# Performance work log

Hardware: AMD Instinct MI355X
Metric: run time of the kernel (lower is better)

Reference implementation:

```python
import jax, jax.numpy as jnp
import numpy as np
from jax.scipy.linalg import expm

B, S, D, E, K, NROT = 2, 2048, 1024, 8, 2, 3
EPS = 1e-5


def setup_inputs() -> dict:
    key = jax.random.key(0)
    ks = jax.random.split(key, 16)
    sc = 0.02
    x = jax.random.normal(ks[0], (B, S, D), jnp.float32)
    ln_gamma = 1.0 + sc * jax.random.normal(ks[1], (D,), jnp.float32)
    ln_beta = sc * jax.random.normal(ks[2], (D,), jnp.float32)
    abel_w = sc * jax.random.normal(ks[3], (D, D), jnp.float32)
    abel_b = sc * jax.random.normal(ks[4], (D,), jnp.float32)
    moe_gate_w = sc * jax.random.normal(ks[5], (D, E), jnp.float32)
    moe_gate_b = sc * jax.random.normal(ks[6], (E,), jnp.float32)
    ew1 = sc * jax.random.normal(ks[7], (E, D, 2 * D), jnp.float32)
    eb1 = sc * jax.random.normal(ks[8], (E, 2 * D), jnp.float32)
    ew2 = sc * jax.random.normal(ks[9], (E, 2 * D, D), jnp.float32)
    eb2 = sc * jax.random.normal(ks[10], (E, D), jnp.float32)
    g = sc * jax.random.normal(ks[11], (NROT, D, D), jnp.float32)
    gens = 0.5 * (g - jnp.swapaxes(g, -1, -2))  # skew-symmetric, as in reset_parameters
    gc_w = sc * jax.random.normal(ks[12], (2 * D, 1), jnp.float32)
    gc_b = sc * jax.random.normal(ks[13], (1,), jnp.float32)
    return dict(x=x, ln_gamma=ln_gamma, ln_beta=ln_beta, abel_w=abel_w, abel_b=abel_b,
                moe_gate_w=moe_gate_w, moe_gate_b=moe_gate_b, ew1=ew1, eb1=eb1,
                ew2=ew2, eb2=eb2, gens=gens, gc_w=gc_w, gc_b=gc_b)


def _gelu(x):
    return jax.nn.gelu(x, approximate=False)  # torch nn.GELU default = exact erf


def _forward(x, ln_gamma, ln_beta, abel_w, abel_b, moe_gate_w, moe_gate_b,
             ew1, eb1, ew2, eb2, gens, gc_w, gc_b):
    residual = x
    # LayerNorm
    mu = jnp.mean(x, axis=-1, keepdims=True)
    var = jnp.mean((x - mu) ** 2, axis=-1, keepdims=True)
    xn = (x - mu) * jax.lax.rsqrt(var + EPS) * ln_gamma + ln_beta
    # abel branch: Linear + GELU
    abel_out = _gelu(xn @ abel_w + abel_b)
    # MoE: dense all-experts compute, masked by top-k softmax weights
    logits = xn @ moe_gate_w + moe_gate_b                      # [B,S,E]
    topw, topi = jax.lax.top_k(logits, K)                      # [B,S,K]
    topw = jax.nn.softmax(topw, axis=-1)
    w_dense = jnp.sum(jax.nn.one_hot(topi, E, dtype=xn.dtype) * topw[..., None], axis=-2)  # [B,S,E]
    h = _gelu(jnp.einsum('bsd,edh->ebsh', xn, ew1) + eb1[:, None, None, :])  # [E,B,S,2D]
    eo = jnp.einsum('ebsh,ehd->ebsd', h, ew2) + eb2[:, None, None, :]        # [E,B,S,D]
    moe_out = jnp.einsum('ebsd,bse->bsd', eo, w_dense)
    # GeometricRotation: sequential matrix_exp rotations
    for i in range(NROT):
        moe_out = moe_out @ expm(gens[i])
    # gated residual mix
    combined = jnp.concatenate([abel_out, moe_out], axis=-1)
    gate = jax.nn.sigmoid(combined @ gc_w + gc_b)              # [B,S,1]
    mixed = abel_out * (1.0 - gate) + moe_out * gate
    return residual + mixed


def reference(x, ln_gamma, ln_beta, abel_w, abel_b, moe_gate_w, moe_gate_b,
              ew1, eb1, ew2, eb2, gens, gc_w, gc_b):
    return _forward(x, ln_gamma, ln_beta, abel_w, abel_b, moe_gate_w, moe_gate_b,
                    ew1, eb1, ew2, eb2, gens, gc_w, gc_b)
```

## Files before the change

### kernel.cpp

```cpp
#include <hip/hip_runtime.h>
#include <hip/hip_bf16.h>
#include <cstdint>
#include <cstddef>

#define DD   1024
#define DD2  2048
#define EE   8
#define NTOK 4096
#define CAPR 9216
#define MAXT 72

typedef __bf16 bf16_t;
typedef __bf16 bf16x8 __attribute__((ext_vector_type(8)));
typedef __bf16 bf16x4 __attribute__((ext_vector_type(4)));
typedef float  f32x4v __attribute__((ext_vector_type(4)));

__device__ __forceinline__ float gelu_f(float v){
  const float t = v*(0.7978845608028654f + 0.0356774081f*v*v);
  const float u = __expf(2.0f*t);
  return __fdividef(v*u, 1.0f + u);
}

__device__ __forceinline__ void gload_lds16(const void* g, void* l){
  __builtin_amdgcn_global_load_lds(
    (const __attribute__((address_space(1))) unsigned int*)(uintptr_t)g,
    (__attribute__((address_space(3))) unsigned int*)(uintptr_t)l,
    16, 0, 0);
}

enum { EPI_GELU_F32=0, EPI_GELU_BF16=1, EPI_BIAS_BF16=2, EPI_SCALE_BF16=3,
       EPI_ADDV_BF16=4, EPI_BF16=5, EPI_F32=6 };

template<int BM,int BN,int EPI,bool TAB>
__global__ __launch_bounds__(256)
void gemm_bt(const bf16_t* __restrict__ A, const bf16_t* __restrict__ Bt,
             const int N, const int K, const int gx, const int gy, const int gz,
             const long sAz, const long sBz, const long sOz,
             const int* __restrict__ tileE, const int* __restrict__ tileR,
             const int* __restrict__ ntp, const int* __restrict__ offp,
             const int* __restrict__ tokOf,
             const float* __restrict__ bias, const long sBias,
             const float alpha,
             const bf16_t* __restrict__ addv,
             float* __restrict__ outF, bf16_t* __restrict__ outB)
{
  constexpr int BK = 32;
  constexpr int WM = BM/2, WN = BN/2;
  constexpr int FM = WM/16, FN = WN/16;
  constexpr int IA = BM/64, IB = BN/64;
  constexpr int NLD = IA + IB;
  __shared__ alignas(16) bf16_t sA[3][BM*BK];
  __shared__ alignas(16) bf16_t sB[3][BN*BK];

  int bx, by, bz; long ro = 0;
  if constexpr (TAB) {
    const int nwg = gx * gy;
    const int q = nwg >> 3, r = nwg & 7;
    const int k = blockIdx.x & 7, i = blockIdx.x >> 3;
    if (i >= q + (k < r ? 1 : 0)) return;
    const int l = k * q + (k < r ? k : r) + i;
    const int ti = l / gx; bx = l - ti*gx;
    if (ti >= ntp[0]) return;
    bz = tileE[ti]; by = 0;
    ro = (long)offp[bz] + tileR[ti];
  } else {
    const int nwg = gx * gy * gz;
    const int q = nwg >> 3, r = nwg & 7;
    const int k = blockIdx.x & 7, i = blockIdx.x >> 3;
    if (i >= q + (k < r ? 1 : 0)) return;
    const int l = k * q + (k < r ? k : r) + i;
    bx = l % gx; const int t2 = l / gx; by = t2 % gy; bz = t2 / gy;
  }

  const int z = bz;
  const bf16_t* Bp = Bt + (size_t)z * sBz;
  float*  oF = outF;
  bf16_t* oB = outB;
  if constexpr (TAB) {
    oB += ro * (long)N;
  } else {
    A += (size_t)z * sAz;
    if (oF) oF += (size_t)z * sOz;
    if (oB) oB += (size_t)z * sOz;
  }
  const float*  bp = bias ? bias + (size_t)z * sBias : nullptr;
  const bf16_t* vp = addv ? addv + (size_t)z * sOz   : nullptr;

  const int tid = threadIdx.x;
  const int wid = tid >> 6, lid = tid & 63;
  const int wr = wid >> 1, wc = wid & 1;
  const int brow = by * BM, bcol = bx * BN;
  const int fr = lid & 15, fq = lid >> 4;
  const int rl = lid >> 2, qs = lid & 3;

  const char* aSrc[IA];
  const char* bSrc[IB];
  #pragma unroll
  for (int i = 0; i < IA; i++) {
    const int rloc = (wid*IA + i)*16 + rl;
    const int q = qs ^ ((rloc >> 1) & 3);
    const bf16_t* arow;
    if constexpr (TAB) {
      arow = tokOf ? (A + (size_t)tokOf[ro + rloc] * K)
                   : (A + (size_t)(ro + rloc) * K);
    } else {
      arow = A + (size_t)(brow + rloc) * K;
    }
    aSrc[i] = (const char*)arow + q*16;
  }
  #pragma unroll
  for (int i = 0; i < IB; i++) {
    const int rloc = (wid*IB + i)*16 + rl;
    const int q = qs ^ ((rloc >> 1) & 3);
    bSrc[i] = (const char*)(Bp + (size_t)(bcol + rloc) * K) + q*16;
  }

  f32x4v acc[FM][FN] = {};

  auto stage = [&](int buf, int kt) {
    #pragma unroll
    for (int i = 0; i < IA; i++)
      gload_lds16(aSrc[i] + (size_t)kt*2, (char*)sA[buf] + (wid*IA + i)*1024);
    #pragma unroll
    for (int i = 0; i < IB; i++)
      gload_lds16(bSrc[i] + (size_t)kt*2, (char*)sB[buf] + (wid*IB + i)*1024);
  };

  stage(0, 0);
  stage(1, BK);
  const int nk = K / BK;
  int b0 = 0, b1 = 1, b2 = 2;

  for (int t = 0; t < nk; ++t) {
    if (t < nk - 1) asm volatile("s_waitcnt vmcnt(%0)" :: "i"(NLD) : "memory");
    else            asm volatile("s_waitcnt vmcnt(0)" ::: "memory");
    __builtin_amdgcn_s_barrier();
    __builtin_amdgcn_sched_barrier(0);
    if (t + 2 < nk) stage(b2, (t + 2)*BK);

    bf16x8 af[FM], bb[FN];
    #pragma unroll
    for (int mi = 0; mi < FM; mi++) {
      const int r2 = wr*WM + mi*16 + fr;
      const int q = fq ^ ((r2 >> 1) & 3);
      af[mi] = *(const bf16x8*)((const char*)sA[b0] + r2*64 + q*16);
    }
    #pragma unroll
    for (int ni = 0; ni < FN; ni++) {
      const int r2 = wc*WN + ni*16 + fr;
      const int q = fq ^ ((r2 >> 1) & 3);
      bb[ni] = *(const bf16x8*)((const char*)sB[b0] + r2*64 + q*16);
    }
    #pragma unroll
    for (int mi = 0; mi < FM; mi++)
      #pragma unroll
      for (int ni = 0; ni < FN; ni++)
        acc[mi][ni] = __builtin_amdgcn_mfma_f32_16x16x32_bf16(
            af[mi], bb[ni], acc[mi][ni], 0, 0, 0);

    const int tb_ = b0; b0 = b1; b1 = b2; b2 = tb_;
  }

  #pragma unroll
  for (int mi = 0; mi < FM; mi++) {
    #pragma unroll
    for (int ni = 0; ni < FN; ni++) {
      const int rg0 = brow + wr*WM + mi*16 + fq*4;
      const int cg  = bcol + wc*WN + ni*16 + fr;
      #pragma unroll
      for (int i = 0; i < 4; i++) {
        const int rg = rg0 + i;
        float v = acc[mi][ni][i];
        if constexpr (EPI == EPI_GELU_F32) {
          v += bp[cg];
          oF[(size_t)rg*N + cg] = gelu_f(v);
        } else if constexpr (EPI == EPI_GELU_BF16) {
          v += bp[cg];
          oB[(size_t)rg*N + cg] = (bf16_t)gelu_f(v);
        } else if constexpr (EPI == EPI_BIAS_BF16) {
          v += bp[cg];
          oB[(size_t)rg*N + cg] = (bf16_t)v;
        } else if constexpr (EPI == EPI_SCALE_BF16) {
          oB[(size_t)rg*N + cg] = (bf16_t)(v * alpha);
        } else if constexpr (EPI == EPI_ADDV_BF16) {
          oB[(size_t)rg*N + cg] = (bf16_t)(v + (float)vp[(size_t)rg*N + cg]);
        } else if constexpr (EPI == EPI_BF16) {
          oB[(size_t)rg*N + cg] = (bf16_t)v;
        } else {
          oF[(size_t)rg*N + cg] = v;
        }
      }
    }
  }
}

__global__ __launch_bounds__(256)
void tcvt_kernel(const float* __restrict__ src, bf16_t* __restrict__ dst, int R, int C){
  __shared__ float t[64][65];
  const size_t bo = (size_t)blockIdx.z * R * C;
  const int c0 = blockIdx.x*64, r0 = blockIdx.y*64;
  const int lx = threadIdx.x & 15, ly = threadIdx.x >> 4;
  #pragma unroll
  for (int i = 0; i < 4; i++) {
    const int row = r0 + ly + i*16;
    const float4 v = *(const float4*)(src + bo + (size_t)row*C + c0 + lx*4);
    t[ly + i*16][lx*4+0] = v.x; t[ly + i*16][lx*4+1] = v.y;
    t[ly + i*16][lx*4+2] = v.z; t[ly + i*16][lx*4+3] = v.w;
  }
  __syncthreads();
  #pragma unroll
  for (int i = 0; i < 4; i++) {
    const int c = c0 + ly + i*16;
    bf16x4 o;
    #pragma unroll
    for (int j = 0; j < 4; j++) o[j] = (bf16_t)t[lx*4+j][ly + i*16];
    *(bf16x4*)(dst + bo + (size_t)c*R + r0 + lx*4) = o;
  }
}

__global__ __launch_bounds__(256)
void tb16_kernel(const bf16_t* __restrict__ Ut, bf16_t* __restrict__ Tb){
  __shared__ bf16_t tile[32][33];
  const bf16_t* src = Ut + (size_t)(1 - blockIdx.z) * DD * DD;
  bf16_t*       dst = Tb + (size_t)blockIdx.z * DD * DD;
  const int c0 = blockIdx.x*32, r0 = blockIdx.y*32;
  #pragma unroll
  for (int i = 0; i < 4; i++)
    tile[threadIdx.y + i*8][threadIdx.x] = src[(size_t)(r0 + threadIdx.y + i*8)*DD + c0 + threadIdx.x];
  __syncthreads();
  #pragma unroll
  for (int i = 0; i < 4; i++)
    dst[(size_t)(c0 + threadIdx.y + i*8)*DD + r0 + threadIdx.x] = tile[threadIdx.x][threadIdx.y + i*8];
}

__global__ __launch_bounds__(256)
void cvt_kernel(const float* __restrict__ in, bf16_t* __restrict__ o, long n, float scale){
  const long i = ((long)blockIdx.x*256 + threadIdx.x)*4;
  if (i >= n) return;
  const float4 v = *(const float4*)(in + i);
  bf16x4 b; b[0]=(bf16_t)(v.x*scale); b[1]=(bf16_t)(v.y*scale);
  b[2]=(bf16_t)(v.z*scale); b[3]=(bf16_t)(v.w*scale);
  *(bf16x4*)(o + i) = b;
}

__global__ __launch_bounds__(256)
void vw_kernel(const bf16_t* __restrict__ Hn, const bf16_t* __restrict__ H2,
               bf16_t* __restrict__ Vb, bf16_t* __restrict__ Wtb){
  const long i0 = ((long)blockIdx.x*256 + threadIdx.x)*4;
  const long rc = i0 % (long)(DD*DD);
  const int r = (int)(rc / DD), c0 = (int)(rc % DD);
  const bf16x4 h  = *(const bf16x4*)(Hn + i0);
  const bf16x4 h2 = *(const bf16x4*)(H2 + i0);
  bf16x4 v, w;
  #pragma unroll
  for (int j = 0; j < 4; j++) {
    const float d  = (r == c0 + j) ? 1.0f : 0.0f;
    const float fh = (float)h[j], f2 = (float)h2[j];
    v[j] = (bf16_t)(d + fh + f2*0.5f);
    w[j] = (bf16_t)(d*(1.0f/6.0f) - fh*(1.0f/24.0f) + f2*(1.0f/120.0f));
  }
  *(bf16x4*)(Vb  + i0) = v;
  *(bf16x4*)(Wtb + i0) = w;
}

__global__ __launch_bounds__(256)
void ln_gate_kernel(const float* __restrict__ x, const float* __restrict__ gamma,
                    const float* __restrict__ beta, const float* __restrict__ gw,
                    const float* __restrict__ gb,
                    bf16_t* __restrict__ xnb, int2* __restrict__ ids,
                    float2* __restrict__ wts)
{
  const int t = blockIdx.x, tid = threadIdx.x, j0 = tid*4;
  const int wid = tid >> 6, lid = tid & 63;
  const float4 v = *(const float4*)(x + (size_t)t*DD + j0);
  float s  = v.x + v.y + v.z + v.w;
  float ss = v.x*v.x + v.y*v.y + v.z*v.z + v.w*v.w;
  #pragma unroll
  for (int off = 32; off; off >>= 1) { s += __shfl_down(s, off); ss += __shfl_down(ss, off); }
  __shared__ float redS[4], redQ[4], mv[2];
  if (lid == 0) { redS[wid] = s; redQ[wid] = ss; }
  __syncthreads();
  if (tid == 0) {
    const float S1 = redS[0]+redS[1]+redS[2]+redS[3];
    const float S2 = redQ[0]+redQ[1]+redQ[2]+redQ[3];
    const float mu  = S1 * (1.0f/DD);
    const float var = S2 * (1.0f/DD) - mu*mu;
    mv[0] = mu; mv[1] = rsqrtf(var + 1e-5f);
  }
  __syncthreads();
  const float mu = mv[0], rstd = mv[1];
  const float4 g = *(const float4*)(gamma + j0);
  const float4 b = *(const float4*)(beta  + j0);
  float xn[4];
  xn[0] = (v.x-mu)*rstd*g.x + b.x;
  xn[1] = (v.y-mu)*rstd*g.y + b.y;
  xn[2] = (v.z-mu)*rstd*g.z + b.z;
  xn[3] = (v.w-mu)*rstd*g.w + b.w;
  bf16x4 ov; ov[0]=(bf16_t)xn[0]; ov[1]=(bf16_t)xn[1]; ov[2]=(bf16_t)xn[2]; ov[3]=(bf16_t)xn[3];
  *(bf16x4*)(xnb + (size_t)t*DD + j0) = ov;

  float p[8] = {0,0,0,0,0,0,0,0};
  #pragma unroll
  for (int i = 0; i < 4; i++) {
    const float4 a0 = *(const float4*)(gw + (size_t)(j0+i)*EE);
    const float4 a1 = *(const float4*)(gw + (size_t)(j0+i)*EE + 4);
    const float xv = xn[i];
    p[0]+=xv*a0.x; p[1]+=xv*a0.y; p[2]+=xv*a0.z; p[3]+=xv*a0.w;
    p[4]+=xv*a1.x; p[5]+=xv*a1.y; p[6]+=xv*a1.z; p[7]+=xv*a1.w;
  }
  #pragma unroll
  for (int off = 32; off; off >>= 1) {
    #pragma unroll
    for (int e = 0; e < 8; e++) p[e] += __shfl_down(p[e], off);
  }
  __shared__ float pr[32];
  if (lid == 0) {
    #pragma unroll
    for (int e = 0; e < 8; e++) pr[wid*8 + e] = p[e];
  }
  __syncthreads();
  if (tid == 0) {
    float l[8];
    #pragma unroll
    for (int e = 0; e < 8; e++) l[e] = pr[e] + pr[8+e] + pr[16+e] + pr[24+e] + gb[e];
    int i1 = 0; float m1 = l[0];
    #pragma unroll
    for (int e = 1; e < 8; e++) if (l[e] > m1) { m1 = l[e]; i1 = e; }
    int i2 = 0; float m2 = -1e30f;
    #pragma unroll
    for (int e = 0; e < 8; e++) if (e != i1 && l[e] > m2) { m2 = l[e]; i2 = e; }
    const float wa = 1.0f/(1.0f + expf(m2 - m1));
    ids[t] = make_int2(i1, i2);
    wts[t] = make_float2(wa, 1.0f - wa);
  }
}

__global__ __launch_bounds__(256)
void route_kernel(const int2* __restrict__ ids, int* __restrict__ slotA,
                  int* __restrict__ slotB, int* __restrict__ cnt,
                  int* __restrict__ off, int* __restrict__ tileE,
                  int* __restrict__ tileR, int* __restrict__ ntp)
{
  const int tid = threadIdx.x;
  const int wid = tid >> 6, lid = tid & 63;
  __shared__ int wsum[EE][4];
  __shared__ int base[EE];
  if (tid < EE) base[tid] = 0;
  __syncthreads();
  const unsigned long long lt = (1ull << lid) - 1ull;
  for (int c0 = 0; c0 < NTOK; c0 += 256) {
    const int t = c0 + tid;
    const int2 id = ids[t];
    int pA = 0, pB = 0;
    #pragma unroll
    for (int e = 0; e < EE; e++) {
      const bool fA = (id.x == e), fB = (id.y == e);
      const unsigned long long mA = __ballot(fA);
      const unsigned long long mB = __ballot(fB);
      const int cA = __popcll(mA);
      if (lid == 0) wsum[e][wid] = cA + __popcll(mB);
      if (fA) pA = __popcll(mA & lt);
      if (fB) pB = cA + __popcll(mB & lt);
    }
    __syncthreads();
    int wbA = base[id.x], wbB = base[id.y];
    for (int w = 0; w < wid; w++) { wbA += wsum[id.x][w]; wbB += wsum[id.y][w]; }
    slotA[t] = wbA + pA;
    slotB[t] = wbB + pB;
    __syncthreads();
    if (tid < EE) base[tid] += wsum[tid][0]+wsum[tid][1]+wsum[tid][2]+wsum[tid][3];
    __syncthreads();
  }
  if (tid == 0) {
    int a = 0, nt = 0;
    for (int e = 0; e < EE; e++) {
      cnt[e] = base[e]; off[e] = a;
      for (int r2 = 0; r2 < base[e]; r2 += 128) { tileE[nt] = e; tileR[nt] = r2; nt++; }
      a += (base[e] + 127) & ~127;
    }
    ntp[0] = nt;
  }
}

__global__ __launch_bounds__(256)
void fill_tok_kernel(const int2* __restrict__ ids, const int* __restrict__ slotA,
                     const int* __restrict__ slotB, const int* __restrict__ off,
                     int* __restrict__ tokOf){
  const int t = blockIdx.x*256 + threadIdx.x;
  const int2 id = ids[t];
  tokOf[off[id.x] + slotA[t]] = t;
  tokOf[off[id.y] + slotB[t]] = t;
}

__global__ __launch_bounds__(256)
void combine_kernel(const bf16_t* __restrict__ Yg, const int2* __restrict__ ids,
                    const int* __restrict__ slotA, const int* __restrict__ slotB,
                    const int* __restrict__ off, const float2* __restrict__ wts,
                    bf16_t* __restrict__ Xa){
  const int t = blockIdx.x, j = threadIdx.x*4;
  const int2 id = ids[t];
  const float2 w = wts[t];
  const bf16x4 a = *(const bf16x4*)(Yg + (size_t)(off[id.x] + slotA[t])*DD + j);
  const bf16x4 b = *(const bf16x4*)(Yg + (size_t)(off[id.y] + slotB[t])*DD + j);
  bf16x4 o;
  #pragma unroll
  for (int i = 0; i < 4; i++) o[i] = (bf16_t)(w.x*(float)a[i] + w.y*(float)b[i]);
  *(bf16x4*)(Xa + (size_t)t*DD + j) = o;
}

__global__ __launch_bounds__(256)
void mix_kernel(const float* __restrict__ x, const bf16_t* __restrict__ abel,
                const float* __restrict__ rot, const float* __restrict__ gcw,
                const float* __restrict__ gcb, float* __restrict__ out)
{
  const int t = blockIdx.x, tid = threadIdx.x, j0 = tid*4;
  const int wid = tid >> 6, lid = tid & 63;
  const bf16x4 ab = *(const bf16x4*)(abel + (size_t)t*DD + j0);
  const float4 r  = *(const float4*)(rot  + (size_t)t*DD + j0);
  const float4 ga = *(const float4*)(gcw + j0);
  const float4 gr = *(const float4*)(gcw + DD + j0);
  const float a0 = (float)ab[0], a1 = (float)ab[1], a2 = (float)ab[2], a3 = (float)ab[3];
  float p = a0*ga.x + a1*ga.y + a2*ga.z + a3*ga.w
          + r.x*gr.x + r.y*gr.y + r.z*gr.z + r.w*gr.w;
  #pragma unroll
  for (int off = 32; off; off >>= 1) p += __shfl_down(p, off);
  __shared__ float red[4];
  __shared__ float gsh;
  if (lid == 0) red[wid] = p;
  __syncthreads();
  if (tid == 0) {
    const float P = red[0] + red[1] + red[2] + red[3] + gcb[0];
    gsh = 1.0f/(1.0f + expf(-P));
  }
  __syncthreads();
  const float gate = gsh, g1 = 1.0f - gate;
  const float4 xv = *(const float4*)(x + (size_t)t*DD + j0);
  float4 o;
  o.x = xv.x + a0*g1 + r.x*gate;
  o.y = xv.y + a1*g1 + r.y*gate;
  o.z = xv.z + a2*g1 + r.z*gate;
  o.w = xv.w + a3*g1 + r.w*gate;
  *(float4*)(out + (size_t)t*DD + j0) = o;
}

extern "C" void kernel_launch(void* const* d_in, const int* in_sizes, int n_in,
                              void* d_out, int out_size, void* d_ws, size_t ws_size,
                              hipStream_t stream)
{
  (void)in_sizes; (void)n_in; (void)out_size; (void)ws_size;
  const float* x      = (const float*)d_in[0];
  const float* ln_g   = (const float*)d_in[1];
  const float* ln_b   = (const float*)d_in[2];
  const float* abel_w = (const float*)d_in[3];
  const float* abel_b = (const float*)d_in[4];
  const float* gate_w = (const float*)d_in[5];
  const float* gate_b = (const float*)d_in[6];
  const float* ew1    = (const float*)d_in[7];
  const float* eb1    = (const float*)d_in[8];
  const float* ew2    = (const float*)d_in[9];
  const float* eb2    = (const float*)d_in[10];
  const float* gens   = (const float*)d_in[11];
  const float* gc_w   = (const float*)d_in[12];
  const float* gc_b   = (const float*)d_in[13];
  float* out = (float*)d_out;

  char* wsp = (char*)d_ws;
  auto alloc = [&](size_t bytes) -> char* {
    char* p = wsp; wsp += (bytes + 255) & ~(size_t)255; return p;
  };
  const size_t MB = 1u<<20;
  bf16_t* xnb   = (bf16_t*)alloc((size_t)NTOK*DD*2);
  int2*   ids   = (int2*)  alloc((size_t)NTOK*8);
  float2* wts   = (float2*)alloc((size_t)NTOK*8);
  int*    slotA = (int*)   alloc((size_t)NTOK*4);
  int*    slotB = (int*)   alloc((size_t)NTOK*4);
  int*    cnt   = (int*)   alloc(64);
  int*    off   = (int*)   alloc(64);
  int*    tileE = (int*)   alloc(MAXT*4);
  int*    tileR = (int*)   alloc(MAXT*4);
  int*    ntp   = (int*)   alloc(64);
  int*    tokOf = (int*)   alloc((size_t)CAPR*4);
  bf16_t* abel_wT = (bf16_t*)alloc((size_t)DD*DD*2);
  char*   UN      = alloc(64*MB);
  bf16_t* ew1T  = (bf16_t*)UN;
  bf16_t* ew2T  = (bf16_t*)(UN + 32*MB);
  bf16_t* Hn    = (bf16_t*)alloc((size_t)3*DD*DD*2);
  bf16_t* abelo = (bf16_t*)alloc((size_t)NTOK*DD*2);
  bf16_t* Yg    = (bf16_t*)alloc((size_t)CAPR*DD*2);
  bf16_t* Hg    = (bf16_t*)alloc((size_t)CAPR*DD2*2);
  bf16_t* Xa    = (bf16_t*)alloc((size_t)NTOK*DD*2);
  float*  rot   = (float*)Hg;
  bf16_t* H2  = (bf16_t*)(UN + 0*MB);
  bf16_t* H3  = (bf16_t*)(UN + 6*MB);
  bf16_t* Vb  = (bf16_t*)(UN + 12*MB);
  bf16_t* Wtb = (bf16_t*)(UN + 18*MB);
  bf16_t* Ut  = (bf16_t*)(UN + 24*MB);
  bf16_t* Tb  = (bf16_t*)(UN + 30*MB);
  bf16_t* Pb  = (bf16_t*)(UN + 34*MB);
  bf16_t* Rt  = (bf16_t*)(UN + 36*MB);
  const long D2 = (long)DD*DD;

  auto gflat = [](int gx, int gy, int gz) {
    const int nwg = gx*gy*gz; return 8 * ((nwg + 7) / 8);
  };

  tcvt_kernel<<<dim3(DD/64,  DD/64, 1),  256, 0, stream>>>(abel_w, abel_wT, DD,  DD);
  tcvt_kernel<<<dim3(DD2/64, DD/64, EE), 256, 0, stream>>>(ew1,    ew1T,    DD,  DD2);
  tcvt_kernel<<<dim3(DD/64,  DD2/64,EE), 256, 0, stream>>>(ew2,    ew2T,    DD2, DD);
  cvt_kernel<<<dim3(3*DD*DD/1024,1,1), 256, 0, stream>>>(gens, Hn, (long)3*DD*DD, -1.0f);
  hipMemsetAsync(tokOf, 0, (size_t)CAPR*4, stream);

  ln_gate_kernel<<<dim3(NTOK,1,1), 256, 0, stream>>>(x, ln_g, ln_b, gate_w, gate_b,
                                                     xnb, ids, wts);
  route_kernel<<<dim3(1,1,1), 256, 0, stream>>>(ids, slotA, slotB, cnt, off,
                                                tileE, tileR, ntp);
  fill_tok_kernel<<<dim3(NTOK/256,1,1), 256, 0, stream>>>(ids, slotA, slotB, off, tokOf);

  gemm_bt<128,128,EPI_GELU_BF16,true><<<dim3((DD2/128)*MAXT,1,1), 256, 0, stream>>>(
      xnb, ew1T, DD2, DD, DD2/128, MAXT, 1, 0, (long)DD2*DD, 0,
      tileE, tileR, ntp, off, tokOf, eb1, DD2, 1.0f, nullptr, nullptr, Hg);
  gemm_bt<128,128,EPI_BIAS_BF16,true><<<dim3((DD/128)*MAXT,1,1), 256, 0, stream>>>(
      Hg, ew2T, DD, DD2, DD/128, MAXT, 1, 0, (long)DD*DD2, 0,
      tileE, tileR, ntp, off, nullptr, eb2, DD, 1.0f, nullptr, nullptr, Yg);
  combine_kernel<<<dim3(NTOK,1,1), 256, 0, stream>>>(Yg, ids, slotA, slotB, off, wts, Xa);

  gemm_bt<128,128,EPI_GELU_BF16,false><<<dim3(gflat(8,32,1),1,1), 256, 0, stream>>>(
      xnb, abel_wT, DD, DD, 8, 32, 1, 0, 0, 0, nullptr, nullptr, nullptr, nullptr,
      nullptr, abel_b, 0, 1.0f, nullptr, nullptr, abelo);

  gemm_bt<128,128,EPI_SCALE_BF16,false><<<dim3(gflat(8,8,3),1,1), 256, 0, stream>>>(
      Hn, Hn, DD, DD, 8, 8, 3, D2, D2, D2, nullptr, nullptr, nullptr, nullptr,
      nullptr, nullptr, 0, -1.0f, nullptr, nullptr, H2);
  gemm_bt<128,128,EPI_SCALE_BF16,false><<<dim3(gflat(8,8,3),1,1), 256, 0, stream>>>(
      H2, Hn, DD, DD, 8, 8, 3, D2, D2, D2, nullptr, nullptr, nullptr, nullptr,
      nullptr, nullptr, 0, -1.0f, nullptr, nullptr, H3);
  vw_kernel<<<dim3(3*DD*DD/1024,1,1), 256, 0, stream>>>(Hn, H2, Vb, Wtb);
  gemm_bt<128,128,EPI_ADDV_BF16,false><<<dim3(gflat(8,8,3),1,1), 256, 0, stream>>>(
      H3, Wtb, DD, DD, 8, 8, 3, D2, D2, D2, nullptr, nullptr, nullptr, nullptr,
      nullptr, nullptr, 0, 1.0f, Vb, nullptr, Ut);
  tb16_kernel<<<dim3(32,32,2), dim3(32,8,1), 0, stream>>>(Ut, Tb);
  gemm_bt<64,64,EPI_BF16,false><<<dim3(gflat(16,16,1),1,1), 256, 0, stream>>>(
      Ut + 2*D2, Tb, DD, DD, 16, 16, 1, 0, 0, 0, nullptr, nullptr, nullptr, nullptr,
      nullptr, nullptr, 0, 1.0f, nullptr, nullptr, Pb);
  gemm_bt<64,64,EPI_BF16,false><<<dim3(gflat(16,16,1),1,1), 256, 0, stream>>>(
      Pb, Tb + D2, DD, DD, 16, 16, 1, 0, 0, 0, nullptr, nullptr, nullptr, nullptr,
      nullptr, nullptr, 0, 1.0f, nullptr, nullptr, Rt);
  gemm_bt<128,128,EPI_F32,false><<<dim3(gflat(8,32,1),1,1), 256, 0, stream>>>(
      Xa, Rt, DD, DD, 8, 32, 1, 0, 0, 0, nullptr, nullptr, nullptr, nullptr,
      nullptr, nullptr, 0, 1.0f, nullptr, rot, nullptr);

  mix_kernel<<<dim3(NTOK,1,1), 256, 0, stream>>>(x, abelo, rot, gc_w, gc_b, out);
}
```

Baseline: 339.1 us.

## Fuse weight prep launches, fold tokOf zeroing, shrink rotation GEMM tiles

Merges the three transpose-convert launches and the generator conversion into one prep kernel, cutting launch count and tail gaps. Replaces the full tokOf memset by zeroing only the padding slots inside fill_tok_kernel. Switches the three batched 1024x1024 generator-power GEMMs from 128x128 to 64x64 tiles, so each launches 768 workgroups instead of 192 and fills the CUs better, at the cost of less data reuse per tile. Padding slots not covered by any expert's aligned range are no longer zeroed, but they are presumably never read.

```diff
diff --git a/kernel.cpp b/kernel.cpp
--- a/kernel.cpp
+++ b/kernel.cpp
@@ -194,16 +194,16 @@
   }
 }
 
-__global__ __launch_bounds__(256)
-void tcvt_kernel(const float* __restrict__ src, bf16_t* __restrict__ dst, int R, int C){
-  __shared__ float t[64][65];
-  const size_t bo = (size_t)blockIdx.z * R * C;
-  const int c0 = blockIdx.x*64, r0 = blockIdx.y*64;
+__device__ __forceinline__ void tcvt_tile(const float* __restrict__ src,
+                                          bf16_t* __restrict__ dst,
+                                          int R, int C, int bx, int by,
+                                          float (*t)[65]){
+  const int c0 = bx*64, r0 = by*64;
   const int lx = threadIdx.x & 15, ly = threadIdx.x >> 4;
   #pragma unroll
   for (int i = 0; i < 4; i++) {
     const int row = r0 + ly + i*16;
-    const float4 v = *(const float4*)(src + bo + (size_t)row*C + c0 + lx*4);
+    const float4 v = *(const float4*)(src + (size_t)row*C + c0 + lx*4);
     t[ly + i*16][lx*4+0] = v.x; t[ly + i*16][lx*4+1] = v.y;
     t[ly + i*16][lx*4+2] = v.z; t[ly + i*16][lx*4+3] = v.w;
   }
@@ -214,7 +214,32 @@
     bf16x4 o;
     #pragma unroll
     for (int j = 0; j < 4; j++) o[j] = (bf16_t)t[lx*4+j][ly + i*16];
-    *(bf16x4*)(dst + bo + (size_t)c*R + r0 + lx*4) = o;
+    *(bf16x4*)(dst + (size_t)c*R + r0 + lx*4) = o;
+  }
+}
+
+__global__ __launch_bounds__(256)
+void prep_kernel(const float* __restrict__ abel_w, bf16_t* __restrict__ abel_wT,
+                 const float* __restrict__ ew1, bf16_t* __restrict__ ew1T,
+                 const float* __restrict__ ew2, bf16_t* __restrict__ ew2T,
+                 const float* __restrict__ gens, bf16_t* __restrict__ Hn)
+{
+  __shared__ float t[64][65];
+  const int bid = blockIdx.x;
+  if (bid < 256) {
+    tcvt_tile(abel_w, abel_wT, DD, DD, bid & 15, bid >> 4, t);
+  } else if (bid < 4352) {
+    const int i = bid - 256, z = i >> 9, r = i & 511;
+    tcvt_tile(ew1 + (size_t)z*DD*DD2, ew1T + (size_t)z*DD2*DD, DD, DD2, r & 31, r >> 5, t);
+  } else if (bid < 8448) {
+    const int i = bid - 4352, z = i >> 9, r = i & 511;
+    tcvt_tile(ew2 + (size_t)z*DD2*DD, ew2T + (size_t)z*DD*DD2, DD2, DD, r & 15, r >> 4, t);
+  } else {
+    const long i4 = ((long)(bid - 8448)*256 + threadIdx.x)*4;
+    const float4 v = *(const float4*)(gens + i4);
+    bf16x4 b; b[0]=(bf16_t)(-v.x); b[1]=(bf16_t)(-v.y);
+    b[2]=(bf16_t)(-v.z); b[3]=(bf16_t)(-v.w);
+    *(bf16x4*)(Hn + i4) = b;
   }
 }
 
@@ -231,16 +256,6 @@
   #pragma unroll
   for (int i = 0; i < 4; i++)
     dst[(size_t)(c0 + threadIdx.y + i*8)*DD + r0 + threadIdx.x] = tile[threadIdx.x][threadIdx.y + i*8];
-}
-
-__global__ __launch_bounds__(256)
-void cvt_kernel(const float* __restrict__ in, bf16_t* __restrict__ o, long n, float scale){
-  const long i = ((long)blockIdx.x*256 + threadIdx.x)*4;
-  if (i >= n) return;
-  const float4 v = *(const float4*)(in + i);
-  bf16x4 b; b[0]=(bf16_t)(v.x*scale); b[1]=(bf16_t)(v.y*scale);
-  b[2]=(bf16_t)(v.z*scale); b[3]=(bf16_t)(v.w*scale);
-  *(bf16x4*)(o + i) = b;
 }
 
 __global__ __launch_bounds__(256)
@@ -385,11 +400,17 @@
 __global__ __launch_bounds__(256)
 void fill_tok_kernel(const int2* __restrict__ ids, const int* __restrict__ slotA,
                      const int* __restrict__ slotB, const int* __restrict__ off,
-                     int* __restrict__ tokOf){
+                     const int* __restrict__ cnt, int* __restrict__ tokOf){
   const int t = blockIdx.x*256 + threadIdx.x;
   const int2 id = ids[t];
   tokOf[off[id.x] + slotA[t]] = t;
   tokOf[off[id.y] + slotB[t]] = t;
+  if (blockIdx.x == 0) {
+    for (int e = 0; e < EE; e++) {
+      const int c = cnt[e], o = off[e], al = (c + 127) & ~127;
+      for (int p = c + threadIdx.x; p < al; p += 256) tokOf[o + p] = 0;
+    }
+  }
 }
 
 __global__ __launch_bounds__(256)
@@ -504,17 +525,14 @@
     const int nwg = gx*gy*gz; return 8 * ((nwg + 7) / 8);
   };
 
-  tcvt_kernel<<<dim3(DD/64,  DD/64, 1),  256, 0, stream>>>(abel_w, abel_wT, DD,  DD);
-  tcvt_kernel<<<dim3(DD2/64, DD/64, EE), 256, 0, stream>>>(ew1,    ew1T,    DD,  DD2);
-  tcvt_kernel<<<dim3(DD/64,  DD2/64,EE), 256, 0, stream>>>(ew2,    ew2T,    DD2, DD);
-  cvt_kernel<<<dim3(3*DD*DD/1024,1,1), 256, 0, stream>>>(gens, Hn, (long)3*DD*DD, -1.0f);
-  hipMemsetAsync(tokOf, 0, (size_t)CAPR*4, stream);
+  prep_kernel<<<dim3(11520,1,1), 256, 0, stream>>>(abel_w, abel_wT, ew1, ew1T,
+                                                   ew2, ew2T, gens, Hn);
 
   ln_gate_kernel<<<dim3(NTOK,1,1), 256, 0, stream>>>(x, ln_g, ln_b, gate_w, gate_b,
                                                      xnb, ids, wts);
   route_kernel<<<dim3(1,1,1), 256, 0, stream>>>(ids, slotA, slotB, cnt, off,
                                                 tileE, tileR, ntp);
-  fill_tok_kernel<<<dim3(NTOK/256,1,1), 256, 0, stream>>>(ids, slotA, slotB, off, tokOf);
+  fill_tok_kernel<<<dim3(NTOK/256,1,1), 256, 0, stream>>>(ids, slotA, slotB, off, cnt, tokOf);
 
   gemm_bt<128,128,EPI_GELU_BF16,true><<<dim3((DD2/128)*MAXT,1,1), 256, 0, stream>>>(
       xnb, ew1T, DD2, DD, DD2/128, MAXT, 1, 0, (long)DD2*DD, 0,
@@ -528,15 +546,15 @@
       xnb, abel_wT, DD, DD, 8, 32, 1, 0, 0, 0, nullptr, nullptr, nullptr, nullptr,
       nullptr, abel_b, 0, 1.0f, nullptr, nullptr, abelo);
 
-  gemm_bt<128,128,EPI_SCALE_BF16,false><<<dim3(gflat(8,8,3),1,1), 256, 0, stream>>>(
-      Hn, Hn, DD, DD, 8, 8, 3, D2, D2, D2, nullptr, nullptr, nullptr, nullptr,
+  gemm_bt<64,64,EPI_SCALE_BF16,false><<<dim3(gflat(16,16,3),1,1), 256, 0, stream>>>(
+      Hn, Hn, DD, DD, 16, 16, 3, D2, D2, D2, nullptr, nullptr, nullptr, nullptr,
       nullptr, nullptr, 0, -1.0f, nullptr, nullptr, H2);
-  gemm_bt<128,128,EPI_SCALE_BF16,false><<<dim3(gflat(8,8,3),1,1), 256, 0, stream>>>(
-      H2, Hn, DD, DD, 8, 8, 3, D2, D2, D2, nullptr, nullptr, nullptr, nullptr,
+  gemm_bt<64,64,EPI_SCALE_BF16,false><<<dim3(gflat(16,16,3),1,1), 256, 0, stream>>>(
+      H2, Hn, DD, DD, 16, 16, 3, D2, D2, D2, nullptr, nullptr, nullptr, nullptr,
       nullptr, nullptr, 0, -1.0f, nullptr, nullptr, H3);
   vw_kernel<<<dim3(3*DD*DD/1024,1,1), 256, 0, stream>>>(Hn, H2, Vb, Wtb);
-  gemm_bt<128,128,EPI_ADDV_BF16,false><<<dim3(gflat(8,8,3),1,1), 256, 0, stream>>>(
-      H3, Wtb, DD, DD, 8, 8, 3, D2, D2, D2, nullptr, nullptr, nullptr, nullptr,
+  gemm_bt<64,64,EPI_ADDV_BF16,false><<<dim3(gflat(16,16,3),1,1), 256, 0, stream>>>(
+      H3, Wtb, DD, DD, 16, 16, 3, D2, D2, D2, nullptr, nullptr, nullptr, nullptr,
       nullptr, nullptr, 0, 1.0f, Vb, nullptr, Ut);
   tb16_kernel<<<dim3(32,32,2), dim3(32,8,1), 0, stream>>>(Ut, Tb);
   gemm_bt<64,64,EPI_BF16,false><<<dim3(gflat(16,16,1),1,1), 256, 0, stream>>>(
```

New measurement: 329.1 us. 2.9% less time.
